# Kernel optimization log

Hardware: AMD Instinct MI355X
Metric: run time of the kernel (lower is better)

Reference implementation:

```python
import jax, jax.numpy as jnp
import numpy as np

B, D, N, MSRC, H = 4, 256, 2048, 2048, 4
DIM = D // H  # per-head dim = 64
EPS = 1e-3


def _conv1x1(W, b, z):
    # 1x1 Conv1d == per-position linear: W [out,in], z [B,in,N]
    return jnp.einsum('oc,bcn->bon', W, z) + b[None, :, None]


def setup_inputs() -> dict:
    key = jax.random.key(0)
    ks = jax.random.split(key, 20)
    s = 0.05
    x = jax.random.normal(ks[0], (B, D, N), dtype=jnp.float32)
    source = jax.random.normal(ks[1], (B, D, MSRC), dtype=jnp.float32)
    mask = (jax.random.uniform(ks[2], (B, N, MSRC)) > 0.3).astype(jnp.float32)
    Wq = jax.random.normal(ks[3], (D, D), jnp.float32) * s
    bq = jax.random.normal(ks[4], (D,), jnp.float32) * s
    Wk = jax.random.normal(ks[5], (D, D), jnp.float32) * s
    bk = jax.random.normal(ks[6], (D,), jnp.float32) * s
    Wv = jax.random.normal(ks[7], (D, D), jnp.float32) * s
    bv = jax.random.normal(ks[8], (D,), jnp.float32) * s
    Wm = jax.random.normal(ks[9], (D, D), jnp.float32) * s
    bm = jax.random.normal(ks[10], (D,), jnp.float32) * s
    W1 = jax.random.normal(ks[11], (2 * D, 2 * D), jnp.float32) * s
    b1 = jax.random.normal(ks[12], (2 * D,), jnp.float32) * s
    gamma = jnp.ones((2 * D,), jnp.float32)
    beta = jnp.zeros((2 * D,), jnp.float32)
    rmean = jax.random.normal(ks[13], (2 * D,), jnp.float32) * 0.1
    rvar = jax.random.uniform(ks[14], (2 * D,), jnp.float32) + 0.5
    W2 = jax.random.normal(ks[15], (D, 2 * D), jnp.float32) * s
    b2 = jnp.zeros((D,), jnp.float32)  # nn.init.constant_(mlp[-1].bias, 0.0)
    return dict(x=x, source=source, mask=mask, Wq=Wq, bq=bq, Wk=Wk, bk=bk,
                Wv=Wv, bv=bv, Wm=Wm, bm=bm, W1=W1, b1=b1, gamma=gamma,
                beta=beta, rmean=rmean, rvar=rvar, W2=W2, b2=b2)


def reference(x, source, mask, Wq, bq, Wk, bk, Wv, bv, Wm, bm,
              W1, b1, gamma, beta, rmean, rvar, W2, b2):
    b = x.shape[0]
    # channel dim split as (dim, heads) per torch .view(B, dim, H, -1)
    q = _conv1x1(Wq, bq, x).reshape(b, DIM, H, -1)        # [B,d,H,N]
    k = _conv1x1(Wk, bk, source).reshape(b, DIM, H, -1)   # [B,d,H,M]
    v = _conv1x1(Wv, bv, source).reshape(b, DIM, H, -1)   # [B,d,H,M]
    scores = jnp.einsum('bdhn,bdhm->bhnm', q, k) / (DIM ** 0.5)
    neg = -jnp.finfo(scores.dtype).max
    scores = jnp.where(mask[:, None, :, :] > 0, scores, neg)
    prob = jax.nn.softmax(scores, axis=-1)                # [B,H,N,M]
    msg = jnp.einsum('bhnm,bdhm->bdhn', prob, v).reshape(b, D, -1)
    message = _conv1x1(Wm, bm, msg)                       # [B,D,N]
    y = jnp.concatenate([x, message], axis=1)             # [B,2D,N]
    h = _conv1x1(W1, b1, y)
    # BatchNorm1d (eval mode, eps=1e-3)
    h = (h - rmean[None, :, None]) * jax.lax.rsqrt(rvar + EPS)[None, :, None]
    h = h * gamma[None, :, None] + beta[None, :, None]
    h = jax.nn.relu(h)
    return _conv1x1(W2, b2, h)                            # [B,D,N]
```

## Files before the change

kernel.cpp:

```cpp
#include <hip/hip_runtime.h>

constexpr int Bb = 4;
constexpr int Dd = 256;
constexpr int Nn = 2048;
constexpr int Mm = 2048;
constexpr int Hh = 4;
constexpr int D2 = 512;
constexpr int NT = Bb * Nn;

#define FMAXV 3.402823466e38f

typedef _Float16 half8 __attribute__((ext_vector_type(8)));
typedef _Float16 half4v __attribute__((ext_vector_type(4)));
typedef _Float16 half2v __attribute__((ext_vector_type(2)));
typedef float f32x4 __attribute__((ext_vector_type(4)));

typedef const __attribute__((address_space(1))) void* gas_p;
typedef __attribute__((address_space(3))) void* las_p;

__device__ __forceinline__ void gload16(const void* g, void* l) {
    __builtin_amdgcn_global_load_lds((gas_p)g, (las_p)l, 16, 0, 0);
}

__global__ __launch_bounds__(256)
void prep_all_kernel(const float* __restrict__ Wq, const float* __restrict__ bq,
                     const float* __restrict__ Wk, const float* __restrict__ bk,
                     const float* __restrict__ Wv, const float* __restrict__ bv,
                     const float* __restrict__ Wm,
                     const float* __restrict__ W1, const float* __restrict__ b1,
                     const float* __restrict__ gamma, const float* __restrict__ beta,
                     const float* __restrict__ rmean, const float* __restrict__ rvar,
                     const float* __restrict__ W2, const float* __restrict__ mask,
                     const float* __restrict__ x, const float* __restrict__ source,
                     _Float16* __restrict__ Wqp, float* __restrict__ bqp,
                     _Float16* __restrict__ Wkvp, float* __restrict__ bkvp,
                     _Float16* __restrict__ Wmp,
                     _Float16* __restrict__ W1p, float* __restrict__ b1f,
                     _Float16* __restrict__ W2p,
                     unsigned long long* __restrict__ bmask,
                     _Float16* __restrict__ Yp, _Float16* __restrict__ Sp) {
    const int r = blockIdx.x, t = threadIdx.x;
    if (r < 256) {
        const int h = r >> 6, d = r & 63, so = d * Hh + h;
        Wqp[r * 256 + t] = (_Float16)Wq[so * 256 + t];
        if (t == 0) bqp[r] = bq[so];
    } else if (r < 768) {
        const int rr = r - 256, part = rr >> 8, o = rr & 255;
        const int h = o >> 6, d = o & 63, so = d * Hh + h;
        const float* Ws = part ? Wv : Wk;
        const float* bs = part ? bv : bk;
        Wkvp[rr * 256 + t] = (_Float16)Ws[so * 256 + t];
        if (t == 0) bkvp[rr] = bs[so];
    } else if (r < 1024) {
        const int o = r - 768;
        const int h = t >> 6, d = t & 63, sk = d * Hh + h;
        Wmp[o * 256 + t] = (_Float16)Wm[o * 256 + sk];
    } else if (r < 1536) {
        const int o = r - 1024;
        const float s = gamma[o] * rsqrtf(rvar[o] + 1e-3f);
        W1p[o * 512 + t]       = (_Float16)(W1[o * 512 + t] * s);
        W1p[o * 512 + t + 256] = (_Float16)(W1[o * 512 + t + 256] * s);
        if (t == 0) b1f[o] = (b1[o] - rmean[o]) * s + beta[o];
    } else if (r < 1792) {
        const int o = r - 1536;
        W2p[o * 512 + t]       = (_Float16)W2[o * 512 + t];
        W2p[o * 512 + t + 256] = (_Float16)W2[o * 512 + t + 256];
    } else if (r < 3840) {
        const int id = r - 1792;
        const int w = t >> 6, lane = t & 63;
        const int row = id * 4 + w;
        const float* mrow = mask + (size_t)row * Mm;
        unsigned long long* brow = bmask + (size_t)row * (Mm / 64);
        #pragma unroll 4
        for (int word = 0; word < Mm / 64; ++word) {
            const float v = mrow[word * 64 + lane];
            const unsigned long long bits = __ballot(v > 0.f);
            if (lane == 0) brow[word] = bits;
        }
    } else {
        __shared__ _Float16 Ts[64][72];
        const int px = r - 3840;
        const int n0 = (px & 31) * 64, c0 = ((px >> 5) & 3) * 64;
        const int z = px >> 7, b = z >> 1, which = z & 1;
        const float* src = which ? source : x;
        _Float16* dst = which ? Sp : Yp;
        const int stride = which ? 256 : 512;
        const int cl = t >> 2, np = (t & 3) * 16;
        const float* sp = src + ((size_t)b * Dd + c0 + cl) * Nn + n0 + np;
        #pragma unroll
        for (int i = 0; i < 4; ++i) {
            float4 v = *(const float4*)(sp + i * 4);
            Ts[np + i * 4 + 0][cl] = (_Float16)v.x;
            Ts[np + i * 4 + 1][cl] = (_Float16)v.y;
            Ts[np + i * 4 + 2][cl] = (_Float16)v.z;
            Ts[np + i * 4 + 3][cl] = (_Float16)v.w;
        }
        __syncthreads();
        const int nl = t >> 2, cp = (t & 3) * 16;
        half8 a0 = *(const half8*)&Ts[nl][cp];
        half8 a1 = *(const half8*)&Ts[nl][cp + 8];
        _Float16* dp = dst + ((size_t)b * Nn + n0 + nl) * stride + c0 + cp;
        *(half8*)dp = a0;
        *(half8*)(dp + 8) = a1;
    }
}

__global__ __launch_bounds__(256)
void gemm4w_kernel(const _Float16* __restrict__ A, const _Float16* __restrict__ A2,
                   const _Float16* __restrict__ W, const float* __restrict__ bias,
                   _Float16* __restrict__ dst0, _Float16* __restrict__ dst1,
                   _Float16* __restrict__ dst2, float* __restrict__ dstF,
                   int K, int sA, int sOut, int modeSel, int relu, float oscale) {
    __shared__ __align__(16) _Float16 As[2 * 128 * 64];
    __shared__ __align__(16) _Float16 Bs[2 * 64 * 64];

    const int t = threadIdx.x;
    const int w = t >> 6, lane = t & 63, quad = lane >> 4, l16 = lane & 15;
    const int n0 = blockIdx.x * 128;
    const int og0 = blockIdx.y * 64;

    int mode = 0, oloc0 = og0;
    const _Float16* Ab = A;
    int sAl = sA;
    _Float16* d0 = dst0;
    float osc = oscale;
    if (modeSel == 3) {
        const int part = blockIdx.y >> 2;
        if (part == 1)      { Ab = A2; sAl = 256; d0 = dst1; oloc0 = og0 - 256; osc = 1.0f; }
        else if (part == 2) { Ab = A2; sAl = 256; mode = 1; oloc0 = og0 - 512; osc = 1.0f; }
    } else if (modeSel == 2) {
        mode = 2;
    }

    const int srow = t >> 3, sslot = t & 7;
    const int schunk = sslot ^ (srow & 7);

    f32x4 acc[2][4] = {};
    const int nk = K / 64;
    int buf = 0;

    {
        #pragma unroll
        for (int c = 0; c < 4; ++c)
            gload16(Ab + (size_t)(n0 + c * 32 + srow) * sAl + schunk * 8,
                    As + c * 2048 + t * 8);
        #pragma unroll
        for (int c = 0; c < 2; ++c)
            gload16(W + (size_t)(og0 + c * 32 + srow) * K + schunk * 8,
                    Bs + c * 2048 + t * 8);
        __asm__ volatile("s_waitcnt vmcnt(0)" ::: "memory");
        __syncthreads();
    }

    #pragma unroll 1
    for (int kt = 0; kt < nk; ++kt) {
        if (kt + 1 < nk) {
            const int k0 = (kt + 1) * 64, nb = buf ^ 1;
            #pragma unroll
            for (int c = 0; c < 4; ++c)
                gload16(Ab + (size_t)(n0 + c * 32 + srow) * sAl + k0 + schunk * 8,
                        As + nb * 8192 + c * 2048 + t * 8);
            #pragma unroll
            for (int c = 0; c < 2; ++c)
                gload16(W + (size_t)(og0 + c * 32 + srow) * K + k0 + schunk * 8,
                        Bs + nb * 4096 + c * 2048 + t * 8);
        }
        #pragma unroll
        for (int ks = 0; ks < 2; ++ks) {
            const int csw = ((ks * 4 + quad) ^ (l16 & 7)) * 8;
            half8 af[2], bf[4];
            #pragma unroll
            for (int i = 0; i < 2; ++i)
                af[i] = *(const half8*)&As[buf * 8192 + (w * 32 + i * 16 + l16) * 64 + csw];
            #pragma unroll
            for (int j = 0; j < 4; ++j)
                bf[j] = *(const half8*)&Bs[buf * 4096 + (j * 16 + l16) * 64 + csw];
            #pragma unroll
            for (int i = 0; i < 2; ++i)
                #pragma unroll
                for (int j = 0; j < 4; ++j)
                    acc[i][j] = __builtin_amdgcn_mfma_f32_16x16x32_f16(af[i], bf[j], acc[i][j], 0, 0, 0);
        }
        if (kt + 1 < nk) {
            __asm__ volatile("s_waitcnt vmcnt(0)" ::: "memory");
            __syncthreads();
            buf ^= 1;
        }
    }

    float bcol[4];
    #pragma unroll
    for (int j = 0; j < 4; ++j) bcol[j] = bias[og0 + j * 16 + l16];

    if (mode == 0) {
        _Float16* Escr = As + w * 2048;
        #pragma unroll
        for (int i = 0; i < 2; ++i) {
            #pragma unroll
            for (int j = 0; j < 4; ++j)
                #pragma unroll
                for (int reg = 0; reg < 4; ++reg) {
                    float v = (acc[i][j][reg] + bcol[j]) * osc;
                    if (relu) v = fmaxf(v, 0.f);
                    Escr[(quad * 4 + reg) * 72 + j * 16 + l16] = (_Float16)v;
                }
            __asm__ volatile("s_waitcnt lgkmcnt(0)" ::: "memory");
            const int row = lane & 15, oseg = (lane >> 4) * 16;
            half8 e0 = *(const half8*)&Escr[row * 72 + oseg];
            half8 e1 = *(const half8*)&Escr[row * 72 + oseg + 8];
            _Float16* dp = d0 + (size_t)(n0 + w * 32 + i * 16 + row) * sOut + oloc0 + oseg;
            *(half8*)dp = e0;
            *(half8*)(dp + 8) = e1;
            __asm__ volatile("s_waitcnt lgkmcnt(0)" ::: "memory");
        }
    } else if (mode == 1) {
        #pragma unroll
        for (int i = 0; i < 2; ++i)
            #pragma unroll
            for (int j = 0; j < 4; ++j) {
                const int c = j * 16 + l16;
                const int mloc = w * 32 + i * 16 + quad * 4;
                const int sw = l16 * 8;
                half4v pv;
                #pragma unroll
                for (int reg = 0; reg < 4; ++reg)
                    pv[reg] = (_Float16)(acc[i][j][reg] + bcol[j]);
                *(half4v*)&As[c * 128 + (mloc ^ sw)] = pv;
            }
        __syncthreads();
        const int n0m = n0 & 2047, bidx = n0 >> 11;
        #pragma unroll
        for (int r = 0; r < 2; ++r) {
            const int c = (t >> 3) + r * 32;
            const int mch = (t & 7) * 16;
            const int sw = (c & 15) * 8;
            half8 v0 = *(const half8*)&As[c * 128 + (mch ^ sw)];
            half8 v1 = *(const half8*)&As[c * 128 + ((mch + 8) ^ sw)];
            _Float16* dp = dst2 + ((size_t)bidx * 256 + oloc0 + c) * (size_t)Mm + n0m + mch;
            *(half8*)dp = v0;
            *(half8*)(dp + 8) = v1;
        }
    } else {
        __syncthreads();
        float* scr = (float*)As;
        #pragma unroll
        for (int i = 0; i < 2; ++i)
            #pragma unroll
            for (int j = 0; j < 4; ++j) {
                const int c = j * 16 + l16;
                const int mloc = w * 32 + i * 16 + quad * 4;
                const int sw = (c & 7) * 4;
                f32x4 v;
                #pragma unroll
                for (int reg = 0; reg < 4; ++reg) v[reg] = acc[i][j][reg] + bcol[j];
                *(f32x4*)&scr[c * 128 + (mloc ^ sw)] = v;
            }
        __syncthreads();
        const int n0m = n0 & 2047, bidx = n0 >> 11;
        #pragma unroll
        for (int r = 0; r < 2; ++r) {
            const int c = (t >> 3) + r * 32;
            const int mch = (t & 7) * 16;
            const int sw = (c & 7) * 4;
            float* dp = dstF + ((size_t)bidx * 256 + og0 + c) * (size_t)Nn + n0m + mch;
            #pragma unroll
            for (int k = 0; k < 4; ++k)
                *(f32x4*)(dp + k * 4) = *(const f32x4*)&scr[c * 128 + ((mch + k * 4) ^ sw)];
        }
    }
}

__global__ __launch_bounds__(256)
void attn_mfma_kernel(const _Float16* __restrict__ Qp, const _Float16* __restrict__ Kp,
                      const _Float16* __restrict__ Vt,
                      const unsigned int* __restrict__ bmask,
                      _Float16* __restrict__ Oa, _Float16* __restrict__ Ob,
                      float* __restrict__ La, float* __restrict__ Lb) {
    __shared__ __align__(16) _Float16 Ks[64][64];
    __shared__ __align__(16) _Float16 Vs[64][64];
    __shared__ __align__(16) _Float16 Ps[4][16][72];

    const int id = blockIdx.x;
    const int xcd = id & 7, loc = id >> 3;
    const int bh = xcd * 2 + (loc >> 6);
    const int sub = loc & 63;
    const int mhalf = sub & 1;
    const int n0 = (sub >> 1) * 64;
    const int b = bh >> 2, h = bh & 3;

    const int t = threadIdx.x;
    const int w = t >> 6, lane = t & 63, quad = lane >> 4, l16 = lane & 15;

    const _Float16* qp = Qp + ((size_t)b * Nn + n0 + w * 16 + l16) * 256 + h * 64 + quad * 8;
    const half8 qa0 = *(const half8*)(qp);
    const half8 qa1 = *(const half8*)(qp + 32);

    const _Float16* Kstg = Kp + (size_t)b * Nn * 256 + h * 64;
    const _Float16* Vstg = Vt + ((size_t)b * 256 + h * 64) * (size_t)Mm;
    const int sr = t >> 2;
    const int sc = (t & 3) * 16;
    const int ss0 = ((t & 3) * 2) ^ (sr & 7);
    const int ss1 = ((t & 3) * 2 + 1) ^ (sr & 7);

    const unsigned int* bmRow = bmask + ((size_t)b * Nn + n0 + w * 16 + l16) * (Mm / 32);

    _Float16* Odst = mhalf ? Ob : Oa;
    float*    Ldst = mhalf ? Lb : La;
    const int mbeg = mhalf * (Mm / 2);

    float psum = 0.f;
    f32x4 O[4] = {};

    half8 sk0, sk1, sv0, sv1;
    auto stage_load = [&](int m0) {
        const _Float16* ks = Kstg + (size_t)(m0 + sr) * 256 + sc;
        sk0 = *(const half8*)(ks);
        sk1 = *(const half8*)(ks + 8);
        const _Float16* vs = Vstg + (size_t)sr * Mm + m0 + sc;
        sv0 = *(const half8*)(vs);
        sv1 = *(const half8*)(vs + 8);
    };
    auto stage_write = [&]() {
        *(half8*)&Ks[sr][ss0 * 8] = sk0;
        *(half8*)&Ks[sr][ss1 * 8] = sk1;
        *(half8*)&Vs[sr][ss0 * 8] = sv0;
        *(half8*)&Vs[sr][ss1 * 8] = sv1;
    };

    stage_load(mbeg);
    stage_write();
    __syncthreads();

    #pragma unroll 1
    for (int it = 0; it < (Mm / 2) / 64; ++it) {
        const int m0 = mbeg + it * 64;
        if (it < (Mm / 2) / 64 - 1) stage_load(m0 + 64);

        const uint2 bmv = *(const uint2*)(bmRow + (m0 >> 5));

        f32x4 S[4];
        #pragma unroll
        for (int mt = 0; mt < 4; ++mt) {
            const int r = mt * 16 + l16, rs = r & 7;
            half8 k0 = *(const half8*)&Ks[r][(quad ^ rs) * 8];
            half8 k1 = *(const half8*)&Ks[r][((quad + 4) ^ rs) * 8];
            f32x4 z = {0.f, 0.f, 0.f, 0.f};
            z = __builtin_amdgcn_mfma_f32_16x16x32_f16(k0, qa0, z, 0, 0, 0);
            z = __builtin_amdgcn_mfma_f32_16x16x32_f16(k1, qa1, z, 0, 0, 0);
            S[mt] = z;
        }

        const unsigned losh = bmv.x >> (quad * 4);
        const unsigned hish = bmv.y >> (quad * 4);
        #pragma unroll
        for (int mt = 0; mt < 4; ++mt) {
            const unsigned wb = (mt < 2) ? losh : hish;
            const int sh = (mt & 1) * 16;
            const float p0 = ((wb >> (sh + 0)) & 1u) ? __builtin_exp2f(S[mt][0]) : 0.f;
            const float p1 = ((wb >> (sh + 1)) & 1u) ? __builtin_exp2f(S[mt][1]) : 0.f;
            const float p2 = ((wb >> (sh + 2)) & 1u) ? __builtin_exp2f(S[mt][2]) : 0.f;
            const float p3 = ((wb >> (sh + 3)) & 1u) ? __builtin_exp2f(S[mt][3]) : 0.f;
            psum += (p0 + p1) + (p2 + p3);
            const half2v lo2 = __builtin_bit_cast(half2v, __builtin_amdgcn_cvt_pkrtz(p0, p1));
            const half2v hi2 = __builtin_bit_cast(half2v, __builtin_amdgcn_cvt_pkrtz(p2, p3));
            half4v pv;
            pv[0] = lo2[0]; pv[1] = lo2[1]; pv[2] = hi2[0]; pv[3] = hi2[1];
            *(half4v*)&Ps[w][l16][mt * 16 + quad * 4] = pv;
        }
        __asm__ volatile("s_waitcnt lgkmcnt(0)" ::: "memory");
        half8 pa0 = *(const half8*)&Ps[w][l16][quad * 8];
        half8 pa1 = *(const half8*)&Ps[w][l16][32 + quad * 8];

        #pragma unroll
        for (int dt = 0; dt < 4; ++dt) {
            const int r = dt * 16 + l16, rs = r & 7;
            half8 v0 = *(const half8*)&Vs[r][(quad ^ rs) * 8];
            half8 v1 = *(const half8*)&Vs[r][((quad + 4) ^ rs) * 8];
            O[dt] = __builtin_amdgcn_mfma_f32_16x16x32_f16(pa0, v0, O[dt], 0, 0, 0);
            O[dt] = __builtin_amdgcn_mfma_f32_16x16x32_f16(pa1, v1, O[dt], 0, 0, 0);
        }

        if (it < (Mm / 2) / 64 - 1) {
            __syncthreads();
            stage_write();
            __syncthreads();
        }
    }

    psum += __shfl_xor(psum, 16);
    psum += __shfl_xor(psum, 32);

    _Float16* op = Odst + ((size_t)b * Nn + n0 + w * 16 + quad * 4) * 256 + h * 64 + l16;
    #pragma unroll
    for (int reg = 0; reg < 4; ++reg)
        #pragma unroll
        for (int dt = 0; dt < 4; ++dt)
            op[(size_t)reg * 256 + dt * 16] = (_Float16)(O[dt][reg] * 0.0625f);
    if (lane < 16)
        Ldst[((size_t)b * Nn + n0 + w * 16 + l16) * 4 + h] = psum * 0.0625f;
}

__global__ __launch_bounds__(256)
void gemm_msg_kernel(const _Float16* __restrict__ Oa, const _Float16* __restrict__ Ob,
                     const float* __restrict__ La, const float* __restrict__ Lb,
                     const _Float16* __restrict__ W, const float* __restrict__ bias,
                     _Float16* __restrict__ dst) {
    __shared__ __align__(16) _Float16 As[2 * 128 * 64];
    __shared__ __align__(16) _Float16 Bs[2 * 64 * 64];

    const int t = threadIdx.x;
    const int w = t >> 6, lane = t & 63, quad = lane >> 4, l16 = lane & 15;
    const int n0 = blockIdx.x * 128;
    const int og0 = blockIdx.y * 64;
    const int srow = t >> 3, sslot = t & 7;
    const int schunk = sslot ^ (srow & 7);
    constexpr int K = 256;

    f32x4 acc[2][4] = {};

    half8 oa[4], ob[4];
    float inv[4];

    auto loadA = [&](int k0) {
        const int h = k0 >> 6;
        #pragma unroll
        for (int c = 0; c < 4; ++c) {
            const size_t row = (size_t)(n0 + c * 32 + srow);
            const size_t off = row * 256 + k0 + schunk * 8;
            oa[c] = *(const half8*)(Oa + off);
            ob[c] = *(const half8*)(Ob + off);
            inv[c] = 1.0f / (La[row * 4 + h] + Lb[row * 4 + h]);
        }
    };
    auto writeA = [&](int nb) {
        #pragma unroll
        for (int c = 0; c < 4; ++c) {
            half8 m;
            #pragma unroll
            for (int k = 0; k < 8; ++k)
                m[k] = (_Float16)(((float)oa[c][k] + (float)ob[c][k]) * inv[c]);
            *(half8*)&As[nb * 8192 + c * 2048 + t * 8] = m;
        }
    };
    auto loadB = [&](int k0, int nb) {
        #pragma unroll
        for (int c = 0; c < 2; ++c)
            gload16(W + (size_t)(og0 + c * 32 + srow) * K + k0 + schunk * 8,
                    Bs + nb * 4096 + c * 2048 + t * 8);
    };

    loadA(0);
    loadB(0, 0);
    writeA(0);
    __asm__ volatile("s_waitcnt vmcnt(0)" ::: "memory");
    __syncthreads();

    int buf = 0;
    #pragma unroll 1
    for (int kt = 0; kt < 4; ++kt) {
        if (kt < 3) {
            loadA((kt + 1) * 64);
            loadB((kt + 1) * 64, buf ^ 1);
        }
        #pragma unroll
        for (int ks = 0; ks < 2; ++ks) {
            const int csw = ((ks * 4 + quad) ^ (l16 & 7)) * 8;
            half8 af[2], bf[4];
            #pragma unroll
            for (int i = 0; i < 2; ++i)
                af[i] = *(const half8*)&As[buf * 8192 + (w * 32 + i * 16 + l16) * 64 + csw];
            #pragma unroll
            for (int j = 0; j < 4; ++j)
                bf[j] = *(const half8*)&Bs[buf * 4096 + (j * 16 + l16) * 64 + csw];
            #pragma unroll
            for (int i = 0; i < 2; ++i)
                #pragma unroll
                for (int j = 0; j < 4; ++j)
                    acc[i][j] = __builtin_amdgcn_mfma_f32_16x16x32_f16(af[i], bf[j], acc[i][j], 0, 0, 0);
        }
        if (kt < 3) {
            writeA(buf ^ 1);
            __asm__ volatile("s_waitcnt vmcnt(0)" ::: "memory");
            __syncthreads();
            buf ^= 1;
        }
    }

    float bcol[4];
    #pragma unroll
    for (int j = 0; j < 4; ++j) bcol[j] = bias[og0 + j * 16 + l16];

    _Float16* Escr = As + w * 2048;
    #pragma unroll
    for (int i = 0; i < 2; ++i) {
        #pragma unroll
        for (int j = 0; j < 4; ++j)
            #pragma unroll
            for (int reg = 0; reg < 4; ++reg)
                Escr[(quad * 4 + reg) * 72 + j * 16 + l16] =
                    (_Float16)(acc[i][j][reg] + bcol[j]);
        __asm__ volatile("s_waitcnt lgkmcnt(0)" ::: "memory");
        const int row = lane & 15, oseg = (lane >> 4) * 16;
        half8 e0 = *(const half8*)&Escr[row * 72 + oseg];
        half8 e1 = *(const half8*)&Escr[row * 72 + oseg + 8];
        _Float16* dp = dst + (size_t)(n0 + w * 32 + i * 16 + row) * 512 + og0 + oseg;
        *(half8*)dp = e0;
        *(half8*)(dp + 8) = e1;
        __asm__ volatile("s_waitcnt lgkmcnt(0)" ::: "memory");
    }
}

extern "C" void kernel_launch(void* const* d_in, const int* in_sizes, int n_in,
                              void* d_out, int out_size, void* d_ws, size_t ws_size,
                              hipStream_t stream) {
    const float* x      = (const float*)d_in[0];
    const float* source = (const float*)d_in[1];
    const float* mask   = (const float*)d_in[2];
    const float* Wq = (const float*)d_in[3];
    const float* bq = (const float*)d_in[4];
    const float* Wk = (const float*)d_in[5];
    const float* bk = (const float*)d_in[6];
    const float* Wv = (const float*)d_in[7];
    const float* bv = (const float*)d_in[8];
    const float* Wm = (const float*)d_in[9];
    const float* bm = (const float*)d_in[10];
    const float* W1 = (const float*)d_in[11];
    const float* b1 = (const float*)d_in[12];
    const float* gamma = (const float*)d_in[13];
    const float* beta  = (const float*)d_in[14];
    const float* rmean = (const float*)d_in[15];
    const float* rvar  = (const float*)d_in[16];
    const float* W2 = (const float*)d_in[17];
    const float* b2 = (const float*)d_in[18];
    float* outp = (float*)d_out;

    char* wsb = (char*)d_ws;
    _Float16* Yp   = (_Float16*)wsb;
    _Float16* Sp   = (_Float16*)(wsb + (8u << 20));
    _Float16* Qp   = (_Float16*)(wsb + (12u << 20));
    _Float16* Kp   = (_Float16*)(wsb + (16u << 20));
    _Float16* Vt   = (_Float16*)(wsb + (20u << 20));
    _Float16* Oa   = (_Float16*)(wsb + (24u << 20));
    _Float16* Hp   = (_Float16*)(wsb + (28u << 20));
    unsigned long long* bmask = (unsigned long long*)(wsb + (28u << 20));
    _Float16* Ob = (_Float16*)(wsb + (30u << 20));
    float* La = (float*)(wsb + (34u << 20));
    float* Lb = (float*)(wsb + (34u << 20) + (128u << 10));
    char* wp = wsb + (36u << 20);
    _Float16* Wqp  = (_Float16*)wp;            wp += 256 * 256 * 2;
    _Float16* Wkvp = (_Float16*)wp;            wp += 512 * 256 * 2;
    _Float16* Wmp  = (_Float16*)wp;            wp += 256 * 256 * 2;
    _Float16* W1p  = (_Float16*)wp;            wp += 512 * 512 * 2;
    _Float16* W2p  = (_Float16*)wp;            wp += 256 * 512 * 2;
    float* bqp  = (float*)wp;                  wp += 256 * 4;
    float* bkvp = (float*)wp;                  wp += 512 * 4;
    float* b1f  = (float*)wp;                  wp += 512 * 4;

    prep_all_kernel<<<4864, 256, 0, stream>>>(
        Wq, bq, Wk, bk, Wv, bv, Wm, W1, b1, gamma, beta, rmean, rvar, W2, mask,
        x, source, Wqp, bqp, Wkvp, bkvp, Wmp, W1p, b1f, W2p, bmask, Yp, Sp);

    gemm4w_kernel<<<dim3(NT / 128, 12), 256, 0, stream>>>(
        Yp, Sp, Wqp, bqp, Qp, Kp, Vt, nullptr, 256, 512, 256, 3, 0, 0.18033688011f);

    attn_mfma_kernel<<<1024, 256, 0, stream>>>(Qp, Kp, Vt,
                                               (const unsigned int*)bmask,
                                               Oa, Ob, La, Lb);

    gemm_msg_kernel<<<dim3(NT / 128, 4), 256, 0, stream>>>(
        Oa, Ob, La, Lb, Wmp, bm, Yp + 256);

    gemm4w_kernel<<<dim3(NT / 128, 8), 256, 0, stream>>>(
        Yp, nullptr, W1p, b1f, Hp, nullptr, nullptr, nullptr, 512, 512, 512, 0, 1, 1.0f);
    gemm4w_kernel<<<dim3(NT / 128, 4), 256, 0, stream>>>(
        Hp, nullptr, W2p, b2, nullptr, nullptr, nullptr, outp, 512, 512, 0, 2, 0, 1.0f);
}
```

Baseline: 239.3 us.

## Split attention key range into quarters with 512-thread blocks sharing K/V tiles

The attention kernel now launches 512-thread blocks (8 waves) covering 128 query rows, and each block handles a quarter of the key range instead of half. Each K/V tile staged in LDS is reused by twice as many waves, and each thread loads one 16-byte chunk per tile instead of two. The message GEMM now merges four partial outputs and four partial sums. Two of the partial buffers reuse the Sp workspace and the output buffer as scratch. This adds extra partial traffic and depends on those buffers being free at that point, but it aims to halve per-block loop length and reduce redundant K/V loads.

```diff
diff --git a/kernel.cpp b/kernel.cpp
--- a/kernel.cpp
+++ b/kernel.cpp
@@ -270,22 +270,24 @@
     }
 }
 
-__global__ __launch_bounds__(256)
+__global__ __launch_bounds__(512, 8)
 void attn_mfma_kernel(const _Float16* __restrict__ Qp, const _Float16* __restrict__ Kp,
                       const _Float16* __restrict__ Vt,
                       const unsigned int* __restrict__ bmask,
                       _Float16* __restrict__ Oa, _Float16* __restrict__ Ob,
-                      float* __restrict__ La, float* __restrict__ Lb) {
+                      _Float16* __restrict__ Oc, _Float16* __restrict__ Od,
+                      float* __restrict__ La, float* __restrict__ Lb,
+                      float* __restrict__ Lc, float* __restrict__ Ld) {
     __shared__ __align__(16) _Float16 Ks[64][64];
     __shared__ __align__(16) _Float16 Vs[64][64];
-    __shared__ __align__(16) _Float16 Ps[4][16][72];
+    __shared__ __align__(16) _Float16 Ps[8][16][72];
 
     const int id = blockIdx.x;
     const int xcd = id & 7, loc = id >> 3;
     const int bh = xcd * 2 + (loc >> 6);
     const int sub = loc & 63;
-    const int mhalf = sub & 1;
-    const int n0 = (sub >> 1) * 64;
+    const int mquart = sub & 3;
+    const int n0 = (sub >> 2) * 128;
     const int b = bh >> 2, h = bh & 3;
 
     const int t = threadIdx.x;
@@ -297,34 +299,27 @@
 
     const _Float16* Kstg = Kp + (size_t)b * Nn * 256 + h * 64;
     const _Float16* Vstg = Vt + ((size_t)b * 256 + h * 64) * (size_t)Mm;
-    const int sr = t >> 2;
-    const int sc = (t & 3) * 16;
-    const int ss0 = ((t & 3) * 2) ^ (sr & 7);
-    const int ss1 = ((t & 3) * 2 + 1) ^ (sr & 7);
+    const int sr = t >> 3;
+    const int sl = t & 7;
+    const int ss = sl ^ (sr & 7);
 
     const unsigned int* bmRow = bmask + ((size_t)b * Nn + n0 + w * 16 + l16) * (Mm / 32);
 
-    _Float16* Odst = mhalf ? Ob : Oa;
-    float*    Ldst = mhalf ? Lb : La;
-    const int mbeg = mhalf * (Mm / 2);
+    _Float16* Odst = mquart == 0 ? Oa : mquart == 1 ? Ob : mquart == 2 ? Oc : Od;
+    float*    Ldst = mquart == 0 ? La : mquart == 1 ? Lb : mquart == 2 ? Lc : Ld;
+    const int mbeg = mquart * (Mm / 4);
 
     float psum = 0.f;
     f32x4 O[4] = {};
 
-    half8 sk0, sk1, sv0, sv1;
+    half8 sk, sv;
     auto stage_load = [&](int m0) {
-        const _Float16* ks = Kstg + (size_t)(m0 + sr) * 256 + sc;
-        sk0 = *(const half8*)(ks);
-        sk1 = *(const half8*)(ks + 8);
-        const _Float16* vs = Vstg + (size_t)sr * Mm + m0 + sc;
-        sv0 = *(const half8*)(vs);
-        sv1 = *(const half8*)(vs + 8);
+        sk = *(const half8*)(Kstg + (size_t)(m0 + sr) * 256 + sl * 8);
+        sv = *(const half8*)(Vstg + (size_t)sr * Mm + m0 + sl * 8);
     };
     auto stage_write = [&]() {
-        *(half8*)&Ks[sr][ss0 * 8] = sk0;
-        *(half8*)&Ks[sr][ss1 * 8] = sk1;
-        *(half8*)&Vs[sr][ss0 * 8] = sv0;
-        *(half8*)&Vs[sr][ss1 * 8] = sv1;
+        *(half8*)&Ks[sr][ss * 8] = sk;
+        *(half8*)&Vs[sr][ss * 8] = sv;
     };
 
     stage_load(mbeg);
@@ -332,9 +327,9 @@
     __syncthreads();
 
     #pragma unroll 1
-    for (int it = 0; it < (Mm / 2) / 64; ++it) {
+    for (int it = 0; it < (Mm / 4) / 64; ++it) {
         const int m0 = mbeg + it * 64;
-        if (it < (Mm / 2) / 64 - 1) stage_load(m0 + 64);
+        if (it < (Mm / 4) / 64 - 1) stage_load(m0 + 64);
 
         const uint2 bmv = *(const uint2*)(bmRow + (m0 >> 5));
 
@@ -380,7 +375,7 @@
             O[dt] = __builtin_amdgcn_mfma_f32_16x16x32_f16(pa1, v1, O[dt], 0, 0, 0);
         }
 
-        if (it < (Mm / 2) / 64 - 1) {
+        if (it < (Mm / 4) / 64 - 1) {
             __syncthreads();
             stage_write();
             __syncthreads();
@@ -402,7 +397,9 @@
 
 __global__ __launch_bounds__(256)
 void gemm_msg_kernel(const _Float16* __restrict__ Oa, const _Float16* __restrict__ Ob,
+                     const _Float16* __restrict__ Oc, const _Float16* __restrict__ Od,
                      const float* __restrict__ La, const float* __restrict__ Lb,
+                     const float* __restrict__ Lc, const float* __restrict__ Ld,
                      const _Float16* __restrict__ W, const float* __restrict__ bias,
                      _Float16* __restrict__ dst) {
     __shared__ __align__(16) _Float16 As[2 * 128 * 64];
@@ -418,7 +415,7 @@
 
     f32x4 acc[2][4] = {};
 
-    half8 oa[4], ob[4];
+    half8 oa[4], ob[4], oc[4], od[4];
     float inv[4];
 
     auto loadA = [&](int k0) {
@@ -429,7 +426,10 @@
             const size_t off = row * 256 + k0 + schunk * 8;
             oa[c] = *(const half8*)(Oa + off);
             ob[c] = *(const half8*)(Ob + off);
-            inv[c] = 1.0f / (La[row * 4 + h] + Lb[row * 4 + h]);
+            oc[c] = *(const half8*)(Oc + off);
+            od[c] = *(const half8*)(Od + off);
+            inv[c] = 1.0f / (La[row * 4 + h] + Lb[row * 4 + h]
+                           + Lc[row * 4 + h] + Ld[row * 4 + h]);
         }
     };
     auto writeA = [&](int nb) {
@@ -438,7 +438,8 @@
             half8 m;
             #pragma unroll
             for (int k = 0; k < 8; ++k)
-                m[k] = (_Float16)(((float)oa[c][k] + (float)ob[c][k]) * inv[c]);
+                m[k] = (_Float16)((((float)oa[c][k] + (float)ob[c][k])
+                                 + ((float)oc[c][k] + (float)od[c][k])) * inv[c]);
             *(half8*)&As[nb * 8192 + c * 2048 + t * 8] = m;
         }
     };
@@ -546,6 +547,10 @@
     _Float16* Ob = (_Float16*)(wsb + (30u << 20));
     float* La = (float*)(wsb + (34u << 20));
     float* Lb = (float*)(wsb + (34u << 20) + (128u << 10));
+    float* Lc = (float*)(wsb + (34u << 20) + (256u << 10));
+    float* Ld = (float*)(wsb + (34u << 20) + (384u << 10));
+    _Float16* Oc = Sp;
+    _Float16* Od = (_Float16*)outp;
     char* wp = wsb + (36u << 20);
     _Float16* Wqp  = (_Float16*)wp;            wp += 256 * 256 * 2;
     _Float16* Wkvp = (_Float16*)wp;            wp += 512 * 256 * 2;
@@ -563,12 +568,12 @@
     gemm4w_kernel<<<dim3(NT / 128, 12), 256, 0, stream>>>(
         Yp, Sp, Wqp, bqp, Qp, Kp, Vt, nullptr, 256, 512, 256, 3, 0, 0.18033688011f);
 
-    attn_mfma_kernel<<<1024, 256, 0, stream>>>(Qp, Kp, Vt,
+    attn_mfma_kernel<<<1024, 512, 0, stream>>>(Qp, Kp, Vt,
                                                (const unsigned int*)bmask,
-                                               Oa, Ob, La, Lb);
+                                               Oa, Ob, Oc, Od, La, Lb, Lc, Ld);
 
     gemm_msg_kernel<<<dim3(NT / 128, 4), 256, 0, stream>>>(
-        Oa, Ob, La, Lb, Wmp, bm, Yp + 256);
+        Oa, Ob, Oc, Od, La, Lb, Lc, Ld, Wmp, bm, Yp + 256);
 
     gemm4w_kernel<<<dim3(NT / 128, 8), 256, 0, stream>>>(
         Yp, nullptr, W1p, b1f, Hp, nullptr, nullptr, nullptr, 512, 512, 512, 0, 1, 1.0f);
```

New measurement: 261.4 us. 1.09x slower.
